# Performance work log

Measured on AMD Instinct MI355X. Metric: run time of the kernel, lower is better.

The kernel has to match this reference:

```python
import jax, jax.numpy as jnp
import numpy as np

N = 10000        # nodes
E = 320000       # edges (before self-loops)
G = 100          # graphs in batch
HEADS = 2
OUT = 125        # per-head out channels
NEG_SLOPE = 0.2  # PyG GATConv default leaky_relu slope


def setup_inputs() -> dict:
    key = jax.random.key(0)
    k = lambda i: jax.random.fold_in(key, i)
    rn = lambda i, shape, s=0.1: jax.random.normal(k(i), shape, jnp.float32) * s
    inp = {
        "x": jax.random.normal(k(0), (N, 336), jnp.float32),
        "edge_index": jax.random.randint(k(1), (2, E), 0, N, jnp.int32),
        "batch": jnp.sort(jax.random.randint(k(2), (N,), 0, G, jnp.int32)),
    }
    conv_in = [336, 250, 250, 250]
    for i, din in enumerate(conv_in, start=1):
        base = 10 * i
        inp[f"W{i}"] = rn(base, (din, HEADS * OUT))
        inp[f"asrc{i}"] = rn(base + 1, (HEADS, OUT))
        inp[f"adst{i}"] = rn(base + 2, (HEADS, OUT))
        inp[f"b{i}"] = jnp.zeros((HEADS * OUT,), jnp.float32)
    lin_dims = [(250, 200), (200, 100), (100, 100), (100, 29)]
    for i, (din, dout) in enumerate(lin_dims, start=1):
        inp[f"lw{i}"] = rn(100 + i, (din, dout))
        inp[f"lb{i}"] = jnp.zeros((dout,), jnp.float32)
    return inp


def gat_conv(x, src, dst, W, asrc, adst, b):
    # PyG GATConv (v1), concat heads, self-loops already in (src, dst).
    n = x.shape[0]
    h = (x @ W).reshape(n, HEADS, OUT)                    # [N,H,C]
    e_src = jnp.einsum('nhc,hc->nh', h, asrc)             # a_src . h_j
    e_dst = jnp.einsum('nhc,hc->nh', h, adst)             # a_dst . h_i
    e = jax.nn.leaky_relu(e_src[src] + e_dst[dst], NEG_SLOPE)  # [Etot,H]
    m = jax.ops.segment_max(e, dst, num_segments=n)       # segment softmax over incoming edges
    e = jnp.exp(e - m[dst])
    denom = jax.ops.segment_sum(e, dst, num_segments=n)
    alpha = e / (denom[dst] + 1e-16)                      # [Etot,H]
    out = jax.ops.segment_sum(alpha[:, :, None] * h[src], dst, num_segments=n)
    return out.reshape(n, HEADS * OUT) + b


def reference(x, edge_index, batch,
              W1, asrc1, adst1, b1, W2, asrc2, adst2, b2,
              W3, asrc3, adst3, b3, W4, asrc4, adst4, b4,
              lw1, lb1, lw2, lb2, lw3, lb3, lw4, lb4):
    n = x.shape[0]
    loop = jnp.arange(n, dtype=edge_index.dtype)
    src = jnp.concatenate([edge_index[0], loop])          # add_self_loops=True
    dst = jnp.concatenate([edge_index[1], loop])

    h = jax.nn.relu(gat_conv(x, src, dst, W1, asrc1, adst1, b1))
    h = jax.nn.relu(gat_conv(h, src, dst, W2, asrc2, adst2, b2))
    h = jax.nn.relu(gat_conv(h, src, dst, W3, asrc3, adst3, b3))
    h = jax.nn.relu(gat_conv(h, src, dst, W4, asrc4, adst4, b4))

    # global_mean_pool over graph ids
    sums = jax.ops.segment_sum(h, batch, num_segments=G)
    cnts = jax.ops.segment_sum(jnp.ones((n, 1), h.dtype), batch, num_segments=G)
    g = sums / jnp.maximum(cnts, 1.0)                     # [G,250]

    g = jax.nn.relu(g @ lw1 + lb1)
    g = jax.nn.relu(g @ lw2 + lb2)
    g = jax.nn.relu(g @ lw3 + lb3)
    return g @ lw4 + lb4                                  # [G,29]
```

## Files before the change

kernel.cpp:

```cpp
#include <hip/hip_runtime.h>
#include <hip/hip_bf16.h>

#define NNODES 10000
#define NEDGES 320000
#define ETOT   (NEDGES + NNODES)
#define NGRAPH 100
#define CH     250
#define HOUT   125
#define MPAD   10048
#define NTILE  157
#define KP0    352
#define KP1    256
#define HPAD   256
#define ECAP   128
#define DCAPW  128

typedef __attribute__((ext_vector_type(8))) short bf16x8;
typedef __attribute__((ext_vector_type(4))) float f32x4;

static __device__ __forceinline__ float bflo(unsigned int u){
  union{ unsigned int i; float f; } v; v.i = u << 16; return v.f;
}
static __device__ __forceinline__ float bfhi(unsigned int u){
  union{ unsigned int i; float f; } v; v.i = u & 0xffff0000u; return v.f;
}
static __device__ __forceinline__ unsigned short f2bfbits(float f){
  __hip_bfloat16 b = __float2bfloat16(f);
  union{ __hip_bfloat16 b; unsigned short s; } v; v.b = b; return v.s;
}

struct Args {
  const float* x; const int* eidx; const int* batch;
  const float *W0,*W1,*W2,*W3;
  __hip_bfloat16 *hb16, *Abf0, *Abf, *Wt0, *Wt1, *Wt2, *Wt3;
  int *cursor; unsigned short* bucket; int *gstart;
};

__global__ void k_pre(Args a){
  int gtid = blockIdx.x * blockDim.x + threadIdx.x;
  int gstr = gridDim.x * blockDim.x;
  for (int e = gtid; e < ETOT; e += gstr){
    int dst, src;
    if (e < NEDGES){ src = a.eidx[e]; dst = a.eidx[NEDGES + e]; }
    else           { src = e - NEDGES; dst = src; }
    int pos = atomicAdd(&a.cursor[dst], 1);
    if (pos < ECAP) a.bucket[(size_t)dst * ECAP + pos] = (unsigned short)src;
  }
  for (int n = gtid; n < NNODES; n += gstr){
    int b1 = a.batch[n];
    int b0 = (n == 0) ? -1 : a.batch[n-1];
    for (int b = b0 + 1; b <= b1; ++b) a.gstart[b] = n;
    if (n == NNODES - 1){
      for (int b = b1 + 1; b <= NGRAPH; ++b) a.gstart[b] = NNODES;
    }
  }
  for (int j = gtid; j < NNODES * 84; j += gstr){
    int r = j / 84, c4 = (j - r * 84) * 4;
    float4 v = *(const float4*)(a.x + (size_t)r * 336 + c4);
    ushort4 o;
    o.x = f2bfbits(v.x); o.y = f2bfbits(v.y); o.z = f2bfbits(v.z); o.w = f2bfbits(v.w);
    *(ushort4*)(a.Abf0 + (size_t)r * KP0 + c4) = o;
  }
  const int T0 = 16 * KP0 * 16;
  const int T1 = 16 * KP1 * 16;
  int tot = T0 + 3*T1;
  for (int i = gtid; i < tot; i += gstr){
    const float* W; __hip_bfloat16* Wt; int K, Kp, li;
    if (i < T0)             { W = a.W0; Wt = a.Wt0; K = 336; Kp = KP0; li = i; }
    else if (i < T0 +   T1) { W = a.W1; Wt = a.Wt1; K = CH;  Kp = KP1; li = i - T0; }
    else if (i < T0 + 2*T1) { W = a.W2; Wt = a.Wt2; K = CH;  Kp = KP1; li = i - T0 - T1; }
    else                    { W = a.W3; Wt = a.Wt3; K = CH;  Kp = KP1; li = i - T0 - 2*T1; }
    int KC = Kp >> 5;
    int nt = li / (Kp * 16);
    int rem = li % (Kp * 16);
    int k = rem / 16;
    int n = rem % 16;
    int col = nt * 16 + n;
    float v = (k < K && col < CH) ? W[(size_t)k * CH + col] : 0.f;
    Wt[(((size_t)nt * KC + (k >> 5)) * 16 + n) * 32 + (k & 31)] = __float2bfloat16(v);
  }
}

__global__ __launch_bounds__(256) void k_gemm(
    const __hip_bfloat16* __restrict__ A, const __hip_bfloat16* __restrict__ Wt,
    __hip_bfloat16* __restrict__ Cb, const float* __restrict__ asrc,
    const float* __restrict__ adst, float* __restrict__ esrc, float* __restrict__ edst,
    int Kp){
  int wv = threadIdx.x >> 6, lane = threadIdx.x & 63;
  int n16 = lane & 15, q = lane >> 4;
  int KC = Kp >> 5;
  int rowbase = blockIdx.x * 64 + wv * 16;
  int bn = blockIdx.y * 64;
  int nt0 = bn >> 4;
  const __hip_bfloat16* ap = A  + (size_t)(rowbase + n16) * Kp + q * 8;
  const __hip_bfloat16* bp = Wt + ((size_t)nt0 * KC * 16 + n16) * 32 + q * 8;
  f32x4 ac0 = {0.f,0.f,0.f,0.f}, ac1 = ac0, ac2 = ac0, ac3 = ac0;
  for (int kc = 0; kc < KC; ++kc){
    bf16x8 a  = *(const bf16x8*)(ap + (size_t)kc * 32);
    bf16x8 b0 = *(const bf16x8*)(bp + ((size_t)0 * KC + kc) * 512);
    bf16x8 b1 = *(const bf16x8*)(bp + ((size_t)1 * KC + kc) * 512);
    bf16x8 b2 = *(const bf16x8*)(bp + ((size_t)2 * KC + kc) * 512);
    bf16x8 b3 = *(const bf16x8*)(bp + ((size_t)3 * KC + kc) * 512);
    ac0 = __builtin_amdgcn_mfma_f32_16x16x32_bf16(a, b0, ac0, 0, 0, 0);
    ac1 = __builtin_amdgcn_mfma_f32_16x16x32_bf16(a, b1, ac1, 0, 0, 0);
    ac2 = __builtin_amdgcn_mfma_f32_16x16x32_bf16(a, b2, ac2, 0, 0, 0);
    ac3 = __builtin_amdgcn_mfma_f32_16x16x32_bf16(a, b3, ac3, 0, 0, 0);
  }
  float es0[4] = {}, es1[4] = {}, ed0a[4] = {}, ed1a[4] = {};
  #define SCORE_T(AC, T) { \
    int col = bn + (T)*16 + n16; \
    bool ok = col < CH; \
    float av = ok ? asrc[col] : 0.f; \
    float dv = ok ? adst[col] : 0.f; \
    bool hh = col >= HOUT; \
    float av0 = hh ? 0.f : av, av1 = hh ? av : 0.f; \
    float dv0 = hh ? 0.f : dv, dv1 = hh ? dv : 0.f; \
    _Pragma("unroll") \
    for (int r = 0; r < 4; ++r){ \
      es0[r] += AC[r]*av0; es1[r] += AC[r]*av1; \
      ed0a[r] += AC[r]*dv0; ed1a[r] += AC[r]*dv1; } }
  SCORE_T(ac0, 0) SCORE_T(ac1, 1) SCORE_T(ac2, 2) SCORE_T(ac3, 3)
  #undef SCORE_T
  #pragma unroll
  for (int off = 1; off < 16; off <<= 1){
    #pragma unroll
    for (int r = 0; r < 4; ++r){
      es0[r]  += __shfl_xor(es0[r],  off);
      es1[r]  += __shfl_xor(es1[r],  off);
      ed0a[r] += __shfl_xor(ed0a[r], off);
      ed1a[r] += __shfl_xor(ed1a[r], off);
    }
  }
  if (n16 == 0){
    #pragma unroll
    for (int r = 0; r < 4; ++r){
      int row = rowbase + q*4 + r;
      if (row < NNODES){
        atomicAdd(&esrc[row*2+0], es0[r]);
        atomicAdd(&esrc[row*2+1], es1[r]);
        atomicAdd(&edst[row*2+0], ed0a[r]);
        atomicAdd(&edst[row*2+1], ed1a[r]);
      }
    }
  }
  #pragma unroll
  for (int r = 0; r < 4; ++r){
    int row = rowbase + q * 4 + r;
    if (row >= NNODES) continue;
    int col = bn + n16;
    __hip_bfloat16* cb = Cb + (size_t)row * HPAD + col;
    cb[0]  = __float2bfloat16(col      < CH ? ac0[r] : 0.f);
    cb[16] = __float2bfloat16(col + 16 < CH ? ac1[r] : 0.f);
    cb[32] = __float2bfloat16(col + 32 < CH ? ac2[r] : 0.f);
    cb[48] = __float2bfloat16(col + 48 < CH ? ac3[r] : 0.f);
  }
}

__global__ __launch_bounds__(256) void k_attn(const __hip_bfloat16* __restrict__ h,
                        const float* __restrict__ esrc, const float* __restrict__ edst,
                        const int* __restrict__ degv, const unsigned short* __restrict__ bucket,
                        const float* __restrict__ bias, __hip_bfloat16* __restrict__ outb,
                        float* __restrict__ esZ, float* __restrict__ edZ){
  int wv = threadIdx.x >> 6, lane = threadIdx.x & 63;
  int node = blockIdx.x * 4 + wv;
  __shared__ int    s_src[4][DCAPW];
  __shared__ float2 s_x[4][DCAPW];
  int deg = degv[node]; if (deg > ECAP) deg = ECAP;
  const unsigned short* __restrict__ eb = bucket + (size_t)node * ECAP;
  float ed0 = edst[node*2+0], ed1 = edst[node*2+1];
  float sm0 = 0.f, sm1 = 0.f;
  for (int i = lane; i < deg; i += 64){
    int src = eb[i];
    float2 ev = *(const float2*)(esrc + (size_t)src * 2);
    float e0 = ev.x + ed0; e0 = e0 > 0.f ? e0 : 0.2f*e0;
    float e1 = ev.y + ed1; e1 = e1 > 0.f ? e1 : 0.2f*e1;
    float x0 = __expf(e0), x1 = __expf(e1);
    s_src[wv][i] = src; s_x[wv][i] = make_float2(x0, x1);
    sm0 += x0; sm1 += x1;
  }
  #pragma unroll
  for (int off = 32; off > 0; off >>= 1){
    sm0 += __shfl_xor(sm0, off);
    sm1 += __shfl_xor(sm1, off);
  }
  float inv0 = 1.f / (sm0 + 1e-16f);
  float inv1 = 1.f / (sm1 + 1e-16f);
  int half = lane >> 5, hl = lane & 31;
  int c0 = hl * 8;
  int n0 = HOUT - c0; n0 = n0 < 0 ? 0 : (n0 > 8 ? 8 : n0);
  const __hip_bfloat16* __restrict__ hrow = h + c0;
  float acc[8] = {0.f,0.f,0.f,0.f,0.f,0.f,0.f,0.f};
  #define EDGE(IDX) { \
    bool vld = (IDX) < deg; \
    int jj = vld ? (IDX) : 0; \
    int s = s_src[wv][jj]; \
    float2 xv = s_x[wv][jj]; \
    float a0 = vld ? xv.x : 0.f; \
    float a1 = vld ? xv.y : 0.f; \
    uint4 d = *(const uint4*)(hrow + (size_t)s * HPAD); \
    acc[0] += (0 < n0 ? a0 : a1) * bflo(d.x); \
    acc[1] += (1 < n0 ? a0 : a1) * bfhi(d.x); \
    acc[2] += (2 < n0 ? a0 : a1) * bflo(d.y); \
    acc[3] += (3 < n0 ? a0 : a1) * bfhi(d.y); \
    acc[4] += (4 < n0 ? a0 : a1) * bflo(d.z); \
    acc[5] += (5 < n0 ? a0 : a1) * bfhi(d.z); \
    acc[6] += (6 < n0 ? a0 : a1) * bflo(d.w); \
    acc[7] += (7 < n0 ? a0 : a1) * bfhi(d.w); }
  for (int it = half; it < deg; it += 8){
    EDGE(it)
    EDGE(it + 2)
    EDGE(it + 4)
    EDGE(it + 6)
  }
  #undef EDGE
  #pragma unroll
  for (int j = 0; j < 8; ++j) acc[j] += __shfl_xor(acc[j], 32);
  if (half == 0){
    if (hl < 31){
      float4 bA = *(const float4*)&bias[c0];
      float4 bB = *(const float4*)&bias[c0 + 4];
      float v0 = acc[0]*(0 < n0 ? inv0 : inv1) + bA.x;
      float v1 = acc[1]*(1 < n0 ? inv0 : inv1) + bA.y;
      float v2 = acc[2]*(2 < n0 ? inv0 : inv1) + bA.z;
      float v3 = acc[3]*(3 < n0 ? inv0 : inv1) + bA.w;
      float v4 = acc[4]*(4 < n0 ? inv0 : inv1) + bB.x;
      float v5 = acc[5]*(5 < n0 ? inv0 : inv1) + bB.y;
      float v6 = acc[6]*(6 < n0 ? inv0 : inv1) + bB.z;
      float v7 = acc[7]*(7 < n0 ? inv0 : inv1) + bB.w;
      v0 = v0 > 0.f ? v0 : 0.f; v1 = v1 > 0.f ? v1 : 0.f;
      v2 = v2 > 0.f ? v2 : 0.f; v3 = v3 > 0.f ? v3 : 0.f;
      v4 = v4 > 0.f ? v4 : 0.f; v5 = v5 > 0.f ? v5 : 0.f;
      v6 = v6 > 0.f ? v6 : 0.f; v7 = v7 > 0.f ? v7 : 0.f;
      uint4 o;
      o.x = (unsigned int)f2bfbits(v0) | ((unsigned int)f2bfbits(v1) << 16);
      o.y = (unsigned int)f2bfbits(v2) | ((unsigned int)f2bfbits(v3) << 16);
      o.z = (unsigned int)f2bfbits(v4) | ((unsigned int)f2bfbits(v5) << 16);
      o.w = (unsigned int)f2bfbits(v6) | ((unsigned int)f2bfbits(v7) << 16);
      *(uint4*)(outb + (size_t)node * KP1 + c0) = o;
    } else {
      float v0 = acc[0]*inv1 + bias[248];
      float v1 = acc[1]*inv1 + bias[249];
      v0 = v0 > 0.f ? v0 : 0.f; v1 = v1 > 0.f ? v1 : 0.f;
      unsigned int o = (unsigned int)f2bfbits(v0) | ((unsigned int)f2bfbits(v1) << 16);
      *(unsigned int*)(outb + (size_t)node * KP1 + 248) = o;
    }
  }
  if (lane < 2){
    esZ[node*2 + lane] = 0.f;
    edZ[node*2 + lane] = 0.f;
  }
}

__global__ __launch_bounds__(256) void k_head(const __hip_bfloat16* __restrict__ xb,
                        const int* __restrict__ gstart,
                        const float* __restrict__ lw1, const float* __restrict__ lb1,
                        const float* __restrict__ lw2, const float* __restrict__ lb2,
                        const float* __restrict__ lw3, const float* __restrict__ lb3,
                        const float* __restrict__ lw4, const float* __restrict__ lb4,
                        float* __restrict__ out){
  int g = blockIdx.x;
  int tid = threadIdx.x;
  int s = gstart[g], e = gstart[g+1];
  __shared__ float gvec[256];
  __shared__ float m1[200];
  __shared__ float m2[112];
  __shared__ float m3[112];
  if (tid < 128){
    int c2 = tid * 2;
    const __hip_bfloat16* xp = xb + c2;
    float a0=0.f,a1=0.f,b0=0.f,b1=0.f;
    int n = s;
    for (; n + 3 < e; n += 4){
      unsigned int u0 = *(const unsigned int*)(xp + (size_t)n     * KP1);
      unsigned int u1 = *(const unsigned int*)(xp + (size_t)(n+1) * KP1);
      unsigned int u2 = *(const unsigned int*)(xp + (size_t)(n+2) * KP1);
      unsigned int u3 = *(const unsigned int*)(xp + (size_t)(n+3) * KP1);
      a0 += bflo(u0) + bflo(u2); a1 += bfhi(u0) + bfhi(u2);
      b0 += bflo(u1) + bflo(u3); b1 += bfhi(u1) + bfhi(u3);
    }
    for (; n < e; ++n){
      unsigned int u0 = *(const unsigned int*)(xp + (size_t)n * KP1);
      a0 += bflo(u0); a1 += bfhi(u0);
    }
    float scale = 1.f / fmaxf((float)(e - s), 1.f);
    gvec[c2]     = (a0 + b0) * scale;
    gvec[c2 + 1] = (a1 + b1) * scale;
  }
  __syncthreads();
  if (tid < 200){
    float a0=0.f,a1=0.f,a2=0.f,a3=0.f;
    int k = 0;
    for (; k + 3 < CH; k += 4){
      a0 += gvec[k]   * lw1[(size_t)k     * 200 + tid];
      a1 += gvec[k+1] * lw1[(size_t)(k+1) * 200 + tid];
      a2 += gvec[k+2] * lw1[(size_t)(k+2) * 200 + tid];
      a3 += gvec[k+3] * lw1[(size_t)(k+3) * 200 + tid];
    }
    for (; k < CH; ++k) a0 += gvec[k] * lw1[(size_t)k * 200 + tid];
    float v = a0 + a1 + a2 + a3 + lb1[tid];
    m1[tid] = v > 0.f ? v : 0.f;
  }
  __syncthreads();
  if (tid < 100){
    float a0=0.f,a1=0.f,a2=0.f,a3=0.f;
    for (int k = 0; k + 3 < 200; k += 4){
      a0 += m1[k]   * lw2[(size_t)k     * 100 + tid];
      a1 += m1[k+1] * lw2[(size_t)(k+1) * 100 + tid];
      a2 += m1[k+2] * lw2[(size_t)(k+2) * 100 + tid];
      a3 += m1[k+3] * lw2[(size_t)(k+3) * 100 + tid];
    }
    float v = a0 + a1 + a2 + a3 + lb2[tid];
    m2[tid] = v > 0.f ? v : 0.f;
  }
  __syncthreads();
  if (tid < 100){
    float a0=0.f,a1=0.f,a2=0.f,a3=0.f;
    for (int k = 0; k + 3 < 100; k += 4){
      a0 += m2[k]   * lw3[(size_t)k     * 100 + tid];
      a1 += m2[k+1] * lw3[(size_t)(k+1) * 100 + tid];
      a2 += m2[k+2] * lw3[(size_t)(k+2) * 100 + tid];
      a3 += m2[k+3] * lw3[(size_t)(k+3) * 100 + tid];
    }
    float v = a0 + a1 + a2 + a3 + lb3[tid];
    m3[tid] = v > 0.f ? v : 0.f;
  }
  __syncthreads();
  if (tid < 29){
    float a0=0.f,a1=0.f,a2=0.f,a3=0.f;
    for (int k = 0; k + 3 < 100; k += 4){
      a0 += m3[k]   * lw4[(size_t)k     * 29 + tid];
      a1 += m3[k+1] * lw4[(size_t)(k+1) * 29 + tid];
      a2 += m3[k+2] * lw4[(size_t)(k+2) * 29 + tid];
      a3 += m3[k+3] * lw4[(size_t)(k+3) * 29 + tid];
    }
    out[(size_t)g * 29 + tid] = a0 + a1 + a2 + a3 + lb4[tid];
  }
}

extern "C" void kernel_launch(void* const* d_in, const int* in_sizes, int n_in,
                              void* d_out, int out_size, void* d_ws, size_t ws_size,
                              hipStream_t stream){
  char* ws = (char*)d_ws;
  size_t off = 0;
  auto alloc = [&](size_t bytes)->void*{
    void* p = ws + off;
    off = (off + bytes + 255) & ~(size_t)255;
    return p;
  };
  __hip_bfloat16* hb16 = (__hip_bfloat16*)alloc((size_t)NNODES * HPAD * 2);
  __hip_bfloat16* Abf0 = (__hip_bfloat16*)alloc((size_t)MPAD * KP0 * 2);
  __hip_bfloat16* Abf  = (__hip_bfloat16*)alloc((size_t)MPAD * KP1 * 2);
  __hip_bfloat16* Wt0  = (__hip_bfloat16*)alloc((size_t)16 * KP0 * 16 * 2);
  __hip_bfloat16* Wt1  = (__hip_bfloat16*)alloc((size_t)16 * KP1 * 16 * 2);
  __hip_bfloat16* Wt2  = (__hip_bfloat16*)alloc((size_t)16 * KP1 * 16 * 2);
  __hip_bfloat16* Wt3  = (__hip_bfloat16*)alloc((size_t)16 * KP1 * 16 * 2);
  size_t zbeg = off;
  int*   cursor = (int*)  alloc((size_t)NNODES * 4);
  float* esA  = (float*)alloc((size_t)NNODES * 2 * 4);
  float* edA  = (float*)alloc((size_t)NNODES * 2 * 4);
  size_t zend = off;
  float* esB  = (float*)alloc((size_t)NNODES * 2 * 4);
  float* edB  = (float*)alloc((size_t)NNODES * 2 * 4);
  unsigned short* bucket = (unsigned short*)alloc((size_t)NNODES * ECAP * 2);
  int*   gstart = (int*)alloc((size_t)(NGRAPH + 1) * 4);

  hipMemsetAsync(ws + zbeg, 0, zend - zbeg, stream);

  Args a;
  a.x = (const float*)d_in[0];
  a.eidx = (const int*)d_in[1];
  a.batch = (const int*)d_in[2];
  a.W0 = (const float*)d_in[3];  a.W1 = (const float*)d_in[7];
  a.W2 = (const float*)d_in[11]; a.W3 = (const float*)d_in[15];
  a.hb16 = hb16; a.Abf0 = Abf0; a.Abf = Abf;
  a.Wt0 = Wt0; a.Wt1 = Wt1; a.Wt2 = Wt2; a.Wt3 = Wt3;
  a.cursor = cursor; a.bucket = bucket; a.gstart = gstart;

  k_pre<<<(ETOT + 255)/256, 256, 0, stream>>>(a);

  const __hip_bfloat16* Wts[4] = {Wt0, Wt1, Wt2, Wt3};
  for (int L = 0; L < 4; ++L){
    const float* as_ = (const float*)d_in[4 + 4*L];
    const float* ad_ = (const float*)d_in[5 + 4*L];
    const float* bb  = (const float*)d_in[6 + 4*L];
    int Kp = (L == 0) ? KP0 : KP1;
    const __hip_bfloat16* Ain = (L == 0) ? Abf0 : Abf;
    float* es  = (L & 1) ? esB : esA;
    float* ed  = (L & 1) ? edB : edA;
    float* esZ = (L & 1) ? esA : esB;
    float* edZ = (L & 1) ? edA : edB;

    k_gemm<<<dim3(NTILE, 4), 256, 0, stream>>>(Ain, Wts[L], hb16, as_, ad_, es, ed, Kp);
    k_attn<<<NNODES/4, 256, 0, stream>>>(hb16, es, ed, cursor, bucket, bb, Abf, esZ, edZ);
  }

  k_head<<<NGRAPH, 256, 0, stream>>>(Abf, gstart,
      (const float*)d_in[19], (const float*)d_in[20],
      (const float*)d_in[21], (const float*)d_in[22],
      (const float*)d_in[23], (const float*)d_in[24],
      (const float*)d_in[25], (const float*)d_in[26],
      (float*)d_out);
}
```

Measured before the change: 293.7 us.

## Fuse attention aggregation of layer L with GEMM of layer L+1

Adds a fused kernel in which each 1024-thread block aggregates attention for 16 nodes, stores the activated bf16 rows in LDS, then multiplies them by the next layer's weights with MFMA and computes the next layer's source and destination attention logits in the block. Layers two to four now run as three fused launches, with ping-pong h buffers, instead of separate GEMM and attention kernels. This removes the global round-trip of the intermediate activations and several launches. In exchange the block size is large, weight tiles are reloaded by every block, and the atomic-free logit reduction goes through LDS. The separate zeroing of the logit buffers is dropped.

```diff
diff --git a/kernel.cpp b/kernel.cpp
--- a/kernel.cpp
+++ b/kernel.cpp
@@ -14,6 +14,7 @@
 #define HPAD   256
 #define ECAP   128
 #define DCAPW  128
+#define APAD   264
 
 typedef __attribute__((ext_vector_type(8))) short bf16x8;
 typedef __attribute__((ext_vector_type(4))) float f32x4;
@@ -32,7 +33,7 @@
 struct Args {
   const float* x; const int* eidx; const int* batch;
   const float *W0,*W1,*W2,*W3;
-  __hip_bfloat16 *hb16, *Abf0, *Abf, *Wt0, *Wt1, *Wt2, *Wt3;
+  __hip_bfloat16 *Abf0, *Wt0, *Wt1, *Wt2, *Wt3;
   int *cursor; unsigned short* bucket; int *gstart;
 };
 
@@ -156,14 +157,173 @@
   }
 }
 
+__global__ __launch_bounds__(1024, 8) void k_fused(
+    const __hip_bfloat16* __restrict__ hcur,
+    const float* __restrict__ esrc, const float* __restrict__ edst,
+    const int* __restrict__ degv, const unsigned short* __restrict__ bucket,
+    const float* __restrict__ bias,
+    const __hip_bfloat16* __restrict__ Wt,
+    const float* __restrict__ asrc, const float* __restrict__ adst,
+    __hip_bfloat16* __restrict__ hnext,
+    float* __restrict__ esN, float* __restrict__ edN){
+  int w = threadIdx.x >> 6, lane = threadIdx.x & 63;
+  int nodebase = blockIdx.x * 16;
+  int node = nodebase + w;
+  __shared__ unsigned short s_src[16][DCAPW];
+  __shared__ float2 s_x[16][DCAPW];
+  __shared__ short  h_lds[16][APAD];
+  __shared__ float  esp[16][16][2];
+  __shared__ float  edp[16][16][2];
+  int deg = degv[node]; if (deg > ECAP) deg = ECAP;
+  const unsigned short* __restrict__ eb = bucket + (size_t)node * ECAP;
+  float ed0 = edst[node*2+0], ed1 = edst[node*2+1];
+  float sm0 = 0.f, sm1 = 0.f;
+  for (int i = lane; i < deg; i += 64){
+    int src = eb[i];
+    float2 ev = *(const float2*)(esrc + (size_t)src * 2);
+    float e0 = ev.x + ed0; e0 = e0 > 0.f ? e0 : 0.2f*e0;
+    float e1 = ev.y + ed1; e1 = e1 > 0.f ? e1 : 0.2f*e1;
+    float x0 = __expf(e0), x1 = __expf(e1);
+    s_src[w][i] = (unsigned short)src; s_x[w][i] = make_float2(x0, x1);
+    sm0 += x0; sm1 += x1;
+  }
+  #pragma unroll
+  for (int off = 32; off > 0; off >>= 1){
+    sm0 += __shfl_xor(sm0, off);
+    sm1 += __shfl_xor(sm1, off);
+  }
+  float inv0 = 1.f / (sm0 + 1e-16f);
+  float inv1 = 1.f / (sm1 + 1e-16f);
+  int half = lane >> 5, hl = lane & 31;
+  int c0 = hl * 8;
+  int n0 = HOUT - c0; n0 = n0 < 0 ? 0 : (n0 > 8 ? 8 : n0);
+  const __hip_bfloat16* __restrict__ hrow = hcur + c0;
+  float acc[8] = {0.f,0.f,0.f,0.f,0.f,0.f,0.f,0.f};
+  #define EDGE(IDX) { \
+    bool vld = (IDX) < deg; \
+    int jj = vld ? (IDX) : 0; \
+    int s = s_src[w][jj]; \
+    float2 xv = s_x[w][jj]; \
+    float a0 = vld ? xv.x : 0.f; \
+    float a1 = vld ? xv.y : 0.f; \
+    uint4 d = *(const uint4*)(hrow + (size_t)s * HPAD); \
+    acc[0] += (0 < n0 ? a0 : a1) * bflo(d.x); \
+    acc[1] += (1 < n0 ? a0 : a1) * bfhi(d.x); \
+    acc[2] += (2 < n0 ? a0 : a1) * bflo(d.y); \
+    acc[3] += (3 < n0 ? a0 : a1) * bfhi(d.y); \
+    acc[4] += (4 < n0 ? a0 : a1) * bflo(d.z); \
+    acc[5] += (5 < n0 ? a0 : a1) * bfhi(d.z); \
+    acc[6] += (6 < n0 ? a0 : a1) * bflo(d.w); \
+    acc[7] += (7 < n0 ? a0 : a1) * bfhi(d.w); }
+  for (int it = half; it < deg; it += 8){
+    EDGE(it)
+    EDGE(it + 2)
+    EDGE(it + 4)
+    EDGE(it + 6)
+  }
+  #undef EDGE
+  #pragma unroll
+  for (int j = 0; j < 8; ++j) acc[j] += __shfl_xor(acc[j], 32);
+  if (half == 0){
+    if (hl < 31){
+      float4 bA = *(const float4*)&bias[c0];
+      float4 bB = *(const float4*)&bias[c0 + 4];
+      float v0 = acc[0]*(0 < n0 ? inv0 : inv1) + bA.x;
+      float v1 = acc[1]*(1 < n0 ? inv0 : inv1) + bA.y;
+      float v2 = acc[2]*(2 < n0 ? inv0 : inv1) + bA.z;
+      float v3 = acc[3]*(3 < n0 ? inv0 : inv1) + bA.w;
+      float v4 = acc[4]*(4 < n0 ? inv0 : inv1) + bB.x;
+      float v5 = acc[5]*(5 < n0 ? inv0 : inv1) + bB.y;
+      float v6 = acc[6]*(6 < n0 ? inv0 : inv1) + bB.z;
+      float v7 = acc[7]*(7 < n0 ? inv0 : inv1) + bB.w;
+      v0 = v0 > 0.f ? v0 : 0.f; v1 = v1 > 0.f ? v1 : 0.f;
+      v2 = v2 > 0.f ? v2 : 0.f; v3 = v3 > 0.f ? v3 : 0.f;
+      v4 = v4 > 0.f ? v4 : 0.f; v5 = v5 > 0.f ? v5 : 0.f;
+      v6 = v6 > 0.f ? v6 : 0.f; v7 = v7 > 0.f ? v7 : 0.f;
+      uint4 o;
+      o.x = (unsigned int)f2bfbits(v0) | ((unsigned int)f2bfbits(v1) << 16);
+      o.y = (unsigned int)f2bfbits(v2) | ((unsigned int)f2bfbits(v3) << 16);
+      o.z = (unsigned int)f2bfbits(v4) | ((unsigned int)f2bfbits(v5) << 16);
+      o.w = (unsigned int)f2bfbits(v6) | ((unsigned int)f2bfbits(v7) << 16);
+      *(uint4*)&h_lds[w][hl*8] = o;
+    } else {
+      float v0 = acc[0]*inv1 + bias[248];
+      float v1 = acc[1]*inv1 + bias[249];
+      v0 = v0 > 0.f ? v0 : 0.f; v1 = v1 > 0.f ? v1 : 0.f;
+      uint4 o;
+      o.x = (unsigned int)f2bfbits(v0) | ((unsigned int)f2bfbits(v1) << 16);
+      o.y = 0u; o.z = 0u; o.w = 0u;
+      *(uint4*)&h_lds[w][248] = o;
+    }
+  }
+  __syncthreads();
+  int n16 = lane & 15, q = lane >> 4;
+  const int KC = KP1 >> 5;
+  const __hip_bfloat16* bp = Wt + ((size_t)w * KC * 16 + n16) * 32 + q * 8;
+  const short* ap = &h_lds[n16][q * 8];
+  f32x4 ac = {0.f,0.f,0.f,0.f};
+  #pragma unroll
+  for (int kc = 0; kc < KC; ++kc){
+    bf16x8 av = *(const bf16x8*)(ap + kc * 32);
+    bf16x8 bv = *(const bf16x8*)(bp + (size_t)kc * 512);
+    ac = __builtin_amdgcn_mfma_f32_16x16x32_bf16(av, bv, ac, 0, 0, 0);
+  }
+  int col = w * 16 + n16;
+  bool ok = col < CH;
+  float av_ = ok ? asrc[col] : 0.f;
+  float dv_ = ok ? adst[col] : 0.f;
+  bool hh = col >= HOUT;
+  float av0 = hh ? 0.f : av_, av1 = hh ? av_ : 0.f;
+  float dv0 = hh ? 0.f : dv_, dv1 = hh ? dv_ : 0.f;
+  float es0[4], es1[4], edd0[4], edd1[4];
+  #pragma unroll
+  for (int r = 0; r < 4; ++r){
+    es0[r] = ac[r]*av0; es1[r] = ac[r]*av1;
+    edd0[r] = ac[r]*dv0; edd1[r] = ac[r]*dv1;
+  }
+  #pragma unroll
+  for (int off = 1; off < 16; off <<= 1){
+    #pragma unroll
+    for (int r = 0; r < 4; ++r){
+      es0[r]  += __shfl_xor(es0[r],  off);
+      es1[r]  += __shfl_xor(es1[r],  off);
+      edd0[r] += __shfl_xor(edd0[r], off);
+      edd1[r] += __shfl_xor(edd1[r], off);
+    }
+  }
+  if (n16 == 0){
+    #pragma unroll
+    for (int r = 0; r < 4; ++r){
+      esp[w][q*4+r][0] = es0[r];  esp[w][q*4+r][1] = es1[r];
+      edp[w][q*4+r][0] = edd0[r]; edp[w][q*4+r][1] = edd1[r];
+    }
+  }
+  #pragma unroll
+  for (int r = 0; r < 4; ++r){
+    int row = nodebase + q*4 + r;
+    hnext[(size_t)row * HPAD + col] = __float2bfloat16(ok ? ac[r] : 0.f);
+  }
+  __syncthreads();
+  int t = threadIdx.x;
+  if (t < 64){
+    int row = t >> 2;
+    int he = t & 1;
+    int which = (t >> 1) & 1;
+    float s = 0.f;
+    #pragma unroll
+    for (int w2 = 0; w2 < 16; ++w2)
+      s += which ? edp[w2][row][he] : esp[w2][row][he];
+    (which ? edN : esN)[(size_t)(nodebase + row) * 2 + he] = s;
+  }
+}
+
 __global__ __launch_bounds__(256) void k_attn(const __hip_bfloat16* __restrict__ h,
                         const float* __restrict__ esrc, const float* __restrict__ edst,
                         const int* __restrict__ degv, const unsigned short* __restrict__ bucket,
-                        const float* __restrict__ bias, __hip_bfloat16* __restrict__ outb,
-                        float* __restrict__ esZ, float* __restrict__ edZ){
+                        const float* __restrict__ bias, __hip_bfloat16* __restrict__ outb){
   int wv = threadIdx.x >> 6, lane = threadIdx.x & 63;
   int node = blockIdx.x * 4 + wv;
-  __shared__ int    s_src[4][DCAPW];
+  __shared__ unsigned short s_src[4][DCAPW];
   __shared__ float2 s_x[4][DCAPW];
   int deg = degv[node]; if (deg > ECAP) deg = ECAP;
   const unsigned short* __restrict__ eb = bucket + (size_t)node * ECAP;
@@ -175,7 +335,7 @@
     float e0 = ev.x + ed0; e0 = e0 > 0.f ? e0 : 0.2f*e0;
     float e1 = ev.y + ed1; e1 = e1 > 0.f ? e1 : 0.2f*e1;
     float x0 = __expf(e0), x1 = __expf(e1);
-    s_src[wv][i] = src; s_x[wv][i] = make_float2(x0, x1);
+    s_src[wv][i] = (unsigned short)src; s_x[wv][i] = make_float2(x0, x1);
     sm0 += x0; sm1 += x1;
   }
   #pragma unroll
@@ -245,10 +405,6 @@
       *(unsigned int*)(outb + (size_t)node * KP1 + 248) = o;
     }
   }
-  if (lane < 2){
-    esZ[node*2 + lane] = 0.f;
-    edZ[node*2 + lane] = 0.f;
-  }
 }
 
 __global__ __launch_bounds__(256) void k_head(const __hip_bfloat16* __restrict__ xb,
@@ -347,7 +503,8 @@
     off = (off + bytes + 255) & ~(size_t)255;
     return p;
   };
-  __hip_bfloat16* hb16 = (__hip_bfloat16*)alloc((size_t)NNODES * HPAD * 2);
+  __hip_bfloat16* hb16A = (__hip_bfloat16*)alloc((size_t)NNODES * HPAD * 2);
+  __hip_bfloat16* hb16B = (__hip_bfloat16*)alloc((size_t)NNODES * HPAD * 2);
   __hip_bfloat16* Abf0 = (__hip_bfloat16*)alloc((size_t)MPAD * KP0 * 2);
   __hip_bfloat16* Abf  = (__hip_bfloat16*)alloc((size_t)MPAD * KP1 * 2);
   __hip_bfloat16* Wt0  = (__hip_bfloat16*)alloc((size_t)16 * KP0 * 16 * 2);
@@ -372,27 +529,27 @@
   a.batch = (const int*)d_in[2];
   a.W0 = (const float*)d_in[3];  a.W1 = (const float*)d_in[7];
   a.W2 = (const float*)d_in[11]; a.W3 = (const float*)d_in[15];
-  a.hb16 = hb16; a.Abf0 = Abf0; a.Abf = Abf;
+  a.Abf0 = Abf0;
   a.Wt0 = Wt0; a.Wt1 = Wt1; a.Wt2 = Wt2; a.Wt3 = Wt3;
   a.cursor = cursor; a.bucket = bucket; a.gstart = gstart;
 
   k_pre<<<(ETOT + 255)/256, 256, 0, stream>>>(a);
 
-  const __hip_bfloat16* Wts[4] = {Wt0, Wt1, Wt2, Wt3};
-  for (int L = 0; L < 4; ++L){
-    const float* as_ = (const float*)d_in[4 + 4*L];
-    const float* ad_ = (const float*)d_in[5 + 4*L];
-    const float* bb  = (const float*)d_in[6 + 4*L];
-    int Kp = (L == 0) ? KP0 : KP1;
-    const __hip_bfloat16* Ain = (L == 0) ? Abf0 : Abf;
-    float* es  = (L & 1) ? esB : esA;
-    float* ed  = (L & 1) ? edB : edA;
-    float* esZ = (L & 1) ? esA : esB;
-    float* edZ = (L & 1) ? edA : edB;
-
-    k_gemm<<<dim3(NTILE, 4), 256, 0, stream>>>(Ain, Wts[L], hb16, as_, ad_, es, ed, Kp);
-    k_attn<<<NNODES/4, 256, 0, stream>>>(hb16, es, ed, cursor, bucket, bb, Abf, esZ, edZ);
-  }
+  k_gemm<<<dim3(NTILE, 4), 256, 0, stream>>>(Abf0, Wt0, hb16A,
+      (const float*)d_in[4], (const float*)d_in[5], esA, edA, KP0);
+
+  k_fused<<<NNODES/16, 1024, 0, stream>>>(hb16A, esA, edA, cursor, bucket,
+      (const float*)d_in[6],  Wt1, (const float*)d_in[8],  (const float*)d_in[9],
+      hb16B, esB, edB);
+  k_fused<<<NNODES/16, 1024, 0, stream>>>(hb16B, esB, edB, cursor, bucket,
+      (const float*)d_in[10], Wt2, (const float*)d_in[12], (const float*)d_in[13],
+      hb16A, esA, edA);
+  k_fused<<<NNODES/16, 1024, 0, stream>>>(hb16A, esA, edA, cursor, bucket,
+      (const float*)d_in[14], Wt3, (const float*)d_in[16], (const float*)d_in[17],
+      hb16B, esB, edB);
+
+  k_attn<<<NNODES/4, 256, 0, stream>>>(hb16B, esB, edB, cursor, bucket,
+      (const float*)d_in[18], Abf);
 
   k_head<<<NGRAPH, 256, 0, stream>>>(Abf, gstart,
       (const float*)d_in[19], (const float*)d_in[20],
```

After: 293.3 us. Within noise of the previous version (-0.2%).
